# Optimization experiments

Measured on AMD Instinct MI355X. Metric: run time of the kernel, lower is better.

The kernel has to match this reference:

```python
import jax, jax.numpy as jnp
import numpy as np

B, N, F, F_PRIME, H = 16, 256, 64, 16, 128  # H = hidden width hardcoded as 128 in source


def _pairwise_dist(r):
    # torch.cdist(r, r), p=2. r: [B,N,3] -> [B,N,N]
    diff = r[:, :, None, :] - r[:, None, :, :]          # [B,N,N,3]
    sq = jnp.sum(diff * diff, axis=-1)                  # [B,N,N]
    safe = jnp.where(sq > 0, sq, 1.0)
    return jnp.where(sq > 0, jnp.sqrt(safe), 0.0)


def setup_inputs() -> dict:
    key = jax.random.key(0)
    ks = jax.random.split(key, 10)
    s = lambda fan_in: 1.0 / np.sqrt(fan_in)
    return {
        "r_batch": jax.random.uniform(ks[0], (B, N, 3), jnp.float32),
        "f_batch": jax.random.uniform(ks[1], (B, N, F), jnp.float32),
        # MessagePassingLayer MLP: 1 -> 128 -> F (weights stored [in, out])
        "mp_w1": jax.random.uniform(ks[2], (1, H), jnp.float32, -s(1), s(1)),
        "mp_b1": jax.random.uniform(ks[3], (H,), jnp.float32, -s(1), s(1)),
        "mp_w2": jax.random.uniform(ks[4], (H, F), jnp.float32, -s(H), s(H)),
        "mp_b2": jax.random.uniform(ks[5], (F,), jnp.float32, -s(H), s(H)),
        # PointwiseConvolutionLayer MLP: F -> 128 -> F_prime
        "pc_w1": jax.random.uniform(ks[6], (F, H), jnp.float32, -s(F), s(F)),
        "pc_b1": jax.random.uniform(ks[7], (H,), jnp.float32, -s(F), s(F)),
        "pc_w2": jax.random.uniform(ks[8], (H, F_PRIME), jnp.float32, -s(H), s(H)),
        "pc_b2": jax.random.uniform(ks[9], (F_PRIME,), jnp.float32, -s(H), s(H)),
    }


def reference(r_batch, f_batch, mp_w1, mp_b1, mp_w2, mp_b2, pc_w1, pc_b1, pc_w2, pc_b2):
    sp = jax.nn.softplus
    d = _pairwise_dist(r_batch)                                   # [B,N,N]
    # per-pair MLP on scalar distance: 1 -> 128 -> F
    hidden = sp(d[..., None] * mp_w1[0] + mp_b1)                  # [B,N,N,H]
    d_prime = sp(jnp.einsum('bijh,hf->bijf', hidden, mp_w2) + mp_b2)  # [B,N,N,F]
    # matmul + diagonal == per-feature weighted sum over neighbors j
    f_bar = sp(jnp.einsum('bijf,bjf->bif', d_prime, f_batch))     # [B,N,F]
    # pointwise MLP: F -> 128 -> F_prime
    h2 = sp(jnp.einsum('bnf,fh->bnh', f_bar, pc_w1) + pc_b1)      # [B,N,H]
    return sp(jnp.einsum('bnh,hp->bnp', h2, pc_w2) + pc_b2)       # [B,N,F_prime]
```

## Files before the change

### kernel.cpp

```cpp
#include <hip/hip_runtime.h>
#include <math.h>

#define B_   16
#define N_   256
#define F_   64
#define FP_  16
#define H_   128
#define K_   14
#define M_   64
#define DMAX 1.7320508075688772f
#define PI_F 3.14159265358979323846f
#define LROW 264
#define HP   136
#define FBP  72
#define MP   72

typedef _Float16 h16;
typedef __attribute__((ext_vector_type(2))) _Float16 h16x2;
typedef __attribute__((ext_vector_type(4))) _Float16 h16x4;
typedef __attribute__((ext_vector_type(8))) _Float16 h16x8;
typedef __attribute__((ext_vector_type(4))) float    f32x4;

__device__ __forceinline__ float sp(float x) {
    return fmaxf(x, 0.0f) + __logf(1.0f + __expf(-fabsf(x)));
}

__global__ __launch_bounds__(512) void pp_fused(
        const float* __restrict__ r,     const float* __restrict__ fb,
        const float* __restrict__ mp_w1, const float* __restrict__ mp_b1,
        const float* __restrict__ mp_w2, const float* __restrict__ mp_b2,
        const float* __restrict__ pc_w1, const float* __restrict__ pc_b1,
        const float* __restrict__ pc_w2, const float* __restrict__ pc_b2,
        float* __restrict__ out) {
    const int tid  = threadIdx.x;
    const int b    = blockIdx.x >> 4;
    const int i0   = (blockIdx.x & 15) << 4;
    const int wv   = tid >> 6;
    const int lane = tid & 63;
    const int ln   = lane & 15;
    const int q    = lane >> 4;

    __shared__ __align__(16) h16 s_hidA[64 * HP];
    __shared__ __align__(16) h16 s_w2T [F_ * HP];
    __shared__ __align__(16) h16 s_valsT[F_ * MP];
    __shared__ __align__(16) h16 s_fbT [F_ * LROW];
    __shared__ __align__(16) h16 s_xs  [16 * LROW];
    __shared__ float s_c  [K_ * F_];
    __shared__ h16   s_w1B[H_ * FBP];
    __shared__ h16   s_w2B[FP_ * HP];
    __shared__ h16   s_fbA[16 * FBP];
    __shared__ h16   s_h2A[16 * HP];
    __shared__ float s_ri [48];
    float* s_part = (float*)s_hidA;

    const int st = tid & 255;
    const int f4 = st & 15;
    const int jp = st >> 4;
    float4 pf0[8], pf1[8];
    float xj = 0.f, yj = 0.f, zj = 0.f;
    if (wv >= 4) {
        const float* fbb = fb + (size_t)b * N_ * F_;
        #pragma unroll
        for (int jb = 0; jb < 8; ++jb) {
            const int j0 = jb * 32 + jp * 2;
            pf0[jb] = *(const float4*)(fbb + (size_t)j0 * F_ + f4 * 4);
            pf1[jb] = *(const float4*)(fbb + (size_t)(j0 + 1) * F_ + f4 * 4);
        }
        xj = r[((size_t)b * N_ + st) * 3 + 0];
        yj = r[((size_t)b * N_ + st) * 3 + 1];
        zj = r[((size_t)b * N_ + st) * 3 + 2];
    }

    if (tid < 48) s_ri[tid] = r[((size_t)b * N_ + i0) * 3 + tid];
    #pragma unroll
    for (int e = 0; e < 4; ++e) {
        const int idx = e * 512 + tid;
        const int f = idx >> 5, h4 = idx & 31;
        const float4 v = *(const float4*)(pc_w1 + f * H_ + h4 * 4);
        s_w1B[(h4 * 4 + 0) * FBP + f] = (h16)v.x;
        s_w1B[(h4 * 4 + 1) * FBP + f] = (h16)v.y;
        s_w1B[(h4 * 4 + 2) * FBP + f] = (h16)v.z;
        s_w1B[(h4 * 4 + 3) * FBP + f] = (h16)v.w;
    }
    #pragma unroll
    for (int e = 0; e < 4; ++e) {
        const int idx = e * 512 + tid;
        const int h = idx >> 4, p = idx & 15;
        s_w2B[p * HP + h] = (h16)pc_w2[idx];
    }
    #pragma unroll
    for (int e = 0; e < 4; ++e) {
        const int idx = e * 512 + tid;
        const int h = idx >> 4, ff4 = idx & 15;
        const float4 v = *(const float4*)(mp_w2 + h * F_ + ff4 * 4);
        s_w2T[(ff4 * 4 + 0) * HP + h] = (h16)v.x;
        s_w2T[(ff4 * 4 + 1) * HP + h] = (h16)v.y;
        s_w2T[(ff4 * 4 + 2) * HP + h] = (h16)v.z;
        s_w2T[(ff4 * 4 + 3) * HP + h] = (h16)v.w;
    }
    {
        const int m  = tid >> 3;
        const int h0 = (tid & 7) * 16;
        const float th = PI_F * ((float)m + 0.5f) / (float)M_;
        const float d  = (__cosf(th) + 1.0f) * 0.5f * DMAX;
        #pragma unroll
        for (int hq = 0; hq < 4; ++hq) {
            const float4 w  = *(const float4*)(mp_w1 + h0 + hq * 4);
            const float4 bb = *(const float4*)(mp_b1 + h0 + hq * 4);
            h16x4 hv;
            hv.x = (h16)sp(fmaf(d, w.x, bb.x));
            hv.y = (h16)sp(fmaf(d, w.y, bb.y));
            hv.z = (h16)sp(fmaf(d, w.z, bb.z));
            hv.w = (h16)sp(fmaf(d, w.w, bb.w));
            *(h16x4*)&s_hidA[m * HP + h0 + hq * 4] = hv;
        }
    }
    __syncthreads();

    if (wv < 4) {
        f32x4 vacc[4];
        #pragma unroll
        for (int ft = 0; ft < 4; ++ft) vacc[ft] = (f32x4){0.f, 0.f, 0.f, 0.f};
        #pragma unroll
        for (int ks = 0; ks < 4; ++ks) {
            const h16x8 af = *(const h16x8*)&s_hidA[(wv * 16 + ln) * HP + ks * 32 + q * 8];
            #pragma unroll
            for (int ft = 0; ft < 4; ++ft) {
                const h16x8 bf = *(const h16x8*)&s_w2T[(ft * 16 + ln) * HP + ks * 32 + q * 8];
                vacc[ft] = __builtin_amdgcn_mfma_f32_16x16x32_f16(af, bf, vacc[ft], 0, 0, 0);
            }
        }
        #pragma unroll
        for (int ft = 0; ft < 4; ++ft) {
            const float b2v = mp_b2[ft * 16 + ln];
            const float vv[4] = {vacc[ft].x, vacc[ft].y, vacc[ft].z, vacc[ft].w};
            #pragma unroll
            for (int rr = 0; rr < 4; ++rr)
                s_valsT[(ft * 16 + ln) * MP + wv * 16 + q * 4 + rr] = (h16)sp(vv[rr] + b2v);
        }
    } else {
        #pragma unroll
        for (int jb = 0; jb < 8; ++jb) {
            const int j0 = jb * 32 + jp * 2;
            const float a0[4] = {pf0[jb].x, pf0[jb].y, pf0[jb].z, pf0[jb].w};
            const float a1[4] = {pf1[jb].x, pf1[jb].y, pf1[jb].z, pf1[jb].w};
            #pragma unroll
            for (int ff = 0; ff < 4; ++ff) {
                h16x2 pk; pk.x = (h16)a0[ff]; pk.y = (h16)a1[ff];
                *(h16x2*)&s_fbT[(f4 * 4 + ff) * LROW + j0] = pk;
            }
        }
    }
    __syncthreads();

    if (wv < 4) {
        f32x4 cacc = (f32x4){0.f, 0.f, 0.f, 0.f};
        #pragma unroll
        for (int cc = 0; cc < 2; ++cc) {
            const h16x8 af = *(const h16x8*)&s_valsT[(wv * 16 + ln) * MP + cc * 32 + q * 8];
            h16x8 bf;
            #pragma unroll
            for (int e = 0; e < 8; ++e) {
                const int m = cc * 32 + q * 8 + e;
                const float th = PI_F * ((float)m + 0.5f) / (float)M_;
                bf[e] = (h16)__cosf((float)ln * th);
            }
            cacc = __builtin_amdgcn_mfma_f32_16x16x32_f16(af, bf, cacc, 0, 0, 0);
        }
        if (ln < K_) {
            const float scale = ((ln == 0) ? 1.0f : 2.0f) / (float)M_;
            const float cv[4] = {cacc.x, cacc.y, cacc.z, cacc.w};
            #pragma unroll
            for (int rr = 0; rr < 4; ++rr)
                s_c[ln * F_ + wv * 16 + q * 4 + rr] = scale * cv[rr];
        }
    } else {
        const float sc = 2.0f / DMAX;
        #pragma unroll
        for (int m = 0; m < 16; ++m) {
            const float dx = s_ri[m * 3 + 0] - xj;
            const float dy = s_ri[m * 3 + 1] - yj;
            const float dz = s_ri[m * 3 + 2] - zj;
            const float sq = fmaf(dx, dx, fmaf(dy, dy, dz * dz));
            const float d  = sq > 0.0f ? sqrtf(sq) : 0.0f;
            s_xs[m * LROW + st] = (h16)(fmaf(d, sc, -1.0f));
        }
    }
    __syncthreads();

    const int j0 = wv * 32 + q * 8;
    const h16x8 x8 = *(const h16x8*)&s_xs[ln * LROW + j0];
    h16x8 bfrag[4];
    #pragma unroll
    for (int ft = 0; ft < 4; ++ft)
        bfrag[ft] = *(const h16x8*)&s_fbT[(ft * 16 + ln) * LROW + j0];

    h16x8 ones, twox, ta, tb;
    #pragma unroll
    for (int e = 0; e < 8; ++e) ones[e] = (h16)1.0f;
    twox = x8 + x8;
    ta = ones;
    tb = x8;

    f32x4 facc[4];
    #pragma unroll
    for (int ft = 0; ft < 4; ++ft) facc[ft] = (f32x4){0.f, 0.f, 0.f, 0.f};
    const f32x4 z4 = (f32x4){0.f, 0.f, 0.f, 0.f};

    for (int k = 0; k < K_; ++k) {
        #pragma unroll
        for (int ft = 0; ft < 4; ++ft) {
            const f32x4 a2 = __builtin_amdgcn_mfma_f32_16x16x32_f16(ta, bfrag[ft], z4, 0, 0, 0);
            const float ck = s_c[k * F_ + ft * 16 + ln];
            facc[ft].x = fmaf(ck, a2.x, facc[ft].x);
            facc[ft].y = fmaf(ck, a2.y, facc[ft].y);
            facc[ft].z = fmaf(ck, a2.z, facc[ft].z);
            facc[ft].w = fmaf(ck, a2.w, facc[ft].w);
        }
        const h16x8 tn = twox * tb - ta;
        ta = tb;
        tb = tn;
    }

    #pragma unroll
    for (int ft = 0; ft < 4; ++ft) {
        const float v[4] = {facc[ft].x, facc[ft].y, facc[ft].z, facc[ft].w};
        #pragma unroll
        for (int rr = 0; rr < 4; ++rr)
            s_part[(wv * 16 + q * 4 + rr) * 68 + ft * 16 + ln] = v[rr];
    }
    __syncthreads();

    #pragma unroll
    for (int e = 0; e < 2; ++e) {
        const int item = e * 512 + tid;
        const int i = item >> 6, f = item & 63;
        float s = 0.0f;
        #pragma unroll
        for (int g = 0; g < 8; ++g)
            s += s_part[(g * 16 + i) * 68 + f];
        s_fbA[i * FBP + f] = (h16)sp(s);
    }
    __syncthreads();

    {
        const int nt = wv;
        f32x4 hacc = (f32x4){0.f, 0.f, 0.f, 0.f};
        #pragma unroll
        for (int ks = 0; ks < 2; ++ks) {
            const h16x8 af = *(const h16x8*)&s_fbA[ln * FBP + ks * 32 + q * 8];
            const h16x8 bf = *(const h16x8*)&s_w1B[(nt * 16 + ln) * FBP + ks * 32 + q * 8];
            hacc = __builtin_amdgcn_mfma_f32_16x16x32_f16(af, bf, hacc, 0, 0, 0);
        }
        const float b1v = pc_b1[nt * 16 + ln];
        const float hv[4] = {hacc.x, hacc.y, hacc.z, hacc.w};
        #pragma unroll
        for (int rr = 0; rr < 4; ++rr)
            s_h2A[(q * 4 + rr) * HP + nt * 16 + ln] = (h16)sp(hv[rr] + b1v);
    }
    __syncthreads();

    {
        f32x4 oacc = (f32x4){0.f, 0.f, 0.f, 0.f};
        #pragma unroll
        for (int ks = 0; ks < 4; ++ks) {
            const h16x8 af = *(const h16x8*)&s_h2A[ln * HP + ks * 32 + q * 8];
            const h16x8 bf = *(const h16x8*)&s_w2B[ln * HP + ks * 32 + q * 8];
            oacc = __builtin_amdgcn_mfma_f32_16x16x32_f16(af, bf, oacc, 0, 0, 0);
        }
        if (wv == 0) {
            const float b2v = pc_b2[ln];
            const float ov[4] = {oacc.x, oacc.y, oacc.z, oacc.w};
            #pragma unroll
            for (int rr = 0; rr < 4; ++rr)
                out[((size_t)(b * N_ + i0 + q * 4 + rr)) * FP_ + ln] = sp(ov[rr] + b2v);
        }
    }
}

extern "C" void kernel_launch(void* const* d_in, const int* in_sizes, int n_in,
                              void* d_out, int out_size, void* d_ws, size_t ws_size,
                              hipStream_t stream) {
    const float* r_batch = (const float*)d_in[0];
    const float* f_batch = (const float*)d_in[1];
    const float* mp_w1   = (const float*)d_in[2];
    const float* mp_b1   = (const float*)d_in[3];
    const float* mp_w2   = (const float*)d_in[4];
    const float* mp_b2   = (const float*)d_in[5];
    const float* pc_w1   = (const float*)d_in[6];
    const float* pc_b1   = (const float*)d_in[7];
    const float* pc_w2   = (const float*)d_in[8];
    const float* pc_b2   = (const float*)d_in[9];
    float* out = (float*)d_out;

    pp_fused<<<B_ * (N_ / 16), 512, 0, stream>>>(
        r_batch, f_batch, mp_w1, mp_b1, mp_w2, mp_b2,
        pc_w1, pc_b1, pc_w2, pc_b2, out);
}
```

Measured before the change: 81.55 us.

## Double block to 1024 threads and split work across sixteen waves

Raises the block size from 512 to 1024 threads and redistributes every stage across 16 wavefronts. Each wave of the Chebyshev MFMA loop now handles 2 feature tiles instead of 4. The value MFMA, f_batch transpose, distance computation and partial-sum reduction are split across more waves. The aim is to shorten the per-block critical path, since the 256 blocks give only about one block per CU. In exchange there are fewer registers per thread, some waves sit idle in certain phases, and synchronising 1024 threads costs more.

```diff
diff --git a/kernel.cpp b/kernel.cpp
--- a/kernel.cpp
+++ b/kernel.cpp
@@ -25,7 +25,7 @@
     return fmaxf(x, 0.0f) + __logf(1.0f + __expf(-fabsf(x)));
 }
 
-__global__ __launch_bounds__(512) void pp_fused(
+__global__ __launch_bounds__(1024) void pp_fused(
         const float* __restrict__ r,     const float* __restrict__ fb,
         const float* __restrict__ mp_w1, const float* __restrict__ mp_b1,
         const float* __restrict__ mp_w2, const float* __restrict__ mp_b2,
@@ -53,28 +53,29 @@
     __shared__ float s_ri [48];
     float* s_part = (float*)s_hidA;
 
-    const int st = tid & 255;
+    const int st = tid & 511;
     const int f4 = st & 15;
     const int jp = st >> 4;
-    float4 pf0[8], pf1[8];
+    float4 pf0[4], pf1[4];
     float xj = 0.f, yj = 0.f, zj = 0.f;
-    if (wv >= 4) {
+    if (wv >= 8) {
         const float* fbb = fb + (size_t)b * N_ * F_;
         #pragma unroll
-        for (int jb = 0; jb < 8; ++jb) {
-            const int j0 = jb * 32 + jp * 2;
+        for (int jb = 0; jb < 4; ++jb) {
+            const int j0 = jb * 64 + jp * 2;
             pf0[jb] = *(const float4*)(fbb + (size_t)j0 * F_ + f4 * 4);
             pf1[jb] = *(const float4*)(fbb + (size_t)(j0 + 1) * F_ + f4 * 4);
         }
-        xj = r[((size_t)b * N_ + st) * 3 + 0];
-        yj = r[((size_t)b * N_ + st) * 3 + 1];
-        zj = r[((size_t)b * N_ + st) * 3 + 2];
+        const int lj = st & 255;
+        xj = r[((size_t)b * N_ + lj) * 3 + 0];
+        yj = r[((size_t)b * N_ + lj) * 3 + 1];
+        zj = r[((size_t)b * N_ + lj) * 3 + 2];
     }
 
     if (tid < 48) s_ri[tid] = r[((size_t)b * N_ + i0) * 3 + tid];
     #pragma unroll
-    for (int e = 0; e < 4; ++e) {
-        const int idx = e * 512 + tid;
+    for (int e = 0; e < 2; ++e) {
+        const int idx = e * 1024 + tid;
         const int f = idx >> 5, h4 = idx & 31;
         const float4 v = *(const float4*)(pc_w1 + f * H_ + h4 * 4);
         s_w1B[(h4 * 4 + 0) * FBP + f] = (h16)v.x;
@@ -83,14 +84,14 @@
         s_w1B[(h4 * 4 + 3) * FBP + f] = (h16)v.w;
     }
     #pragma unroll
-    for (int e = 0; e < 4; ++e) {
-        const int idx = e * 512 + tid;
+    for (int e = 0; e < 2; ++e) {
+        const int idx = e * 1024 + tid;
         const int h = idx >> 4, p = idx & 15;
         s_w2B[p * HP + h] = (h16)pc_w2[idx];
     }
     #pragma unroll
-    for (int e = 0; e < 4; ++e) {
-        const int idx = e * 512 + tid;
+    for (int e = 0; e < 2; ++e) {
+        const int idx = e * 1024 + tid;
         const int h = idx >> 4, ff4 = idx & 15;
         const float4 v = *(const float4*)(mp_w2 + h * F_ + ff4 * 4);
         s_w2T[(ff4 * 4 + 0) * HP + h] = (h16)v.x;
@@ -99,12 +100,12 @@
         s_w2T[(ff4 * 4 + 3) * HP + h] = (h16)v.w;
     }
     {
-        const int m  = tid >> 3;
-        const int h0 = (tid & 7) * 16;
+        const int m  = tid >> 4;
+        const int h0 = (tid & 15) * 8;
         const float th = PI_F * ((float)m + 0.5f) / (float)M_;
         const float d  = (__cosf(th) + 1.0f) * 0.5f * DMAX;
         #pragma unroll
-        for (int hq = 0; hq < 4; ++hq) {
+        for (int hq = 0; hq < 2; ++hq) {
             const float4 w  = *(const float4*)(mp_w1 + h0 + hq * 4);
             const float4 bb = *(const float4*)(mp_b1 + h0 + hq * 4);
             h16x4 hv;
@@ -117,31 +118,34 @@
     }
     __syncthreads();
 
-    if (wv < 4) {
-        f32x4 vacc[4];
-        #pragma unroll
-        for (int ft = 0; ft < 4; ++ft) vacc[ft] = (f32x4){0.f, 0.f, 0.f, 0.f};
+    if (wv < 8) {
+        const int mt = wv & 3, fg = wv >> 2;
+        f32x4 vacc[2];
+        #pragma unroll
+        for (int t = 0; t < 2; ++t) vacc[t] = (f32x4){0.f, 0.f, 0.f, 0.f};
         #pragma unroll
         for (int ks = 0; ks < 4; ++ks) {
-            const h16x8 af = *(const h16x8*)&s_hidA[(wv * 16 + ln) * HP + ks * 32 + q * 8];
-            #pragma unroll
-            for (int ft = 0; ft < 4; ++ft) {
+            const h16x8 af = *(const h16x8*)&s_hidA[(mt * 16 + ln) * HP + ks * 32 + q * 8];
+            #pragma unroll
+            for (int t = 0; t < 2; ++t) {
+                const int ft = fg * 2 + t;
                 const h16x8 bf = *(const h16x8*)&s_w2T[(ft * 16 + ln) * HP + ks * 32 + q * 8];
-                vacc[ft] = __builtin_amdgcn_mfma_f32_16x16x32_f16(af, bf, vacc[ft], 0, 0, 0);
+                vacc[t] = __builtin_amdgcn_mfma_f32_16x16x32_f16(af, bf, vacc[t], 0, 0, 0);
             }
         }
         #pragma unroll
-        for (int ft = 0; ft < 4; ++ft) {
+        for (int t = 0; t < 2; ++t) {
+            const int ft = fg * 2 + t;
             const float b2v = mp_b2[ft * 16 + ln];
-            const float vv[4] = {vacc[ft].x, vacc[ft].y, vacc[ft].z, vacc[ft].w};
+            const float vv[4] = {vacc[t].x, vacc[t].y, vacc[t].z, vacc[t].w};
             #pragma unroll
             for (int rr = 0; rr < 4; ++rr)
-                s_valsT[(ft * 16 + ln) * MP + wv * 16 + q * 4 + rr] = (h16)sp(vv[rr] + b2v);
+                s_valsT[(ft * 16 + ln) * MP + mt * 16 + q * 4 + rr] = (h16)sp(vv[rr] + b2v);
         }
     } else {
         #pragma unroll
-        for (int jb = 0; jb < 8; ++jb) {
-            const int j0 = jb * 32 + jp * 2;
+        for (int jb = 0; jb < 4; ++jb) {
+            const int j0 = jb * 64 + jp * 2;
             const float a0[4] = {pf0[jb].x, pf0[jb].y, pf0[jb].z, pf0[jb].w};
             const float a1[4] = {pf1[jb].x, pf1[jb].y, pf1[jb].z, pf1[jb].w};
             #pragma unroll
@@ -174,26 +178,30 @@
             for (int rr = 0; rr < 4; ++rr)
                 s_c[ln * F_ + wv * 16 + q * 4 + rr] = scale * cv[rr];
         }
-    } else {
+    } else if (wv >= 8) {
+        const int lj   = st & 255;
+        const int half = st >> 8;
         const float sc = 2.0f / DMAX;
         #pragma unroll
-        for (int m = 0; m < 16; ++m) {
+        for (int mm = 0; mm < 8; ++mm) {
+            const int m = half * 8 + mm;
             const float dx = s_ri[m * 3 + 0] - xj;
             const float dy = s_ri[m * 3 + 1] - yj;
             const float dz = s_ri[m * 3 + 2] - zj;
             const float sq = fmaf(dx, dx, fmaf(dy, dy, dz * dz));
             const float d  = sq > 0.0f ? sqrtf(sq) : 0.0f;
-            s_xs[m * LROW + st] = (h16)(fmaf(d, sc, -1.0f));
-        }
-    }
-    __syncthreads();
-
-    const int j0 = wv * 32 + q * 8;
+            s_xs[m * LROW + lj] = (h16)(fmaf(d, sc, -1.0f));
+        }
+    }
+    __syncthreads();
+
+    const int jw = wv & 7, fg = wv >> 3;
+    const int j0 = jw * 32 + q * 8;
     const h16x8 x8 = *(const h16x8*)&s_xs[ln * LROW + j0];
-    h16x8 bfrag[4];
-    #pragma unroll
-    for (int ft = 0; ft < 4; ++ft)
-        bfrag[ft] = *(const h16x8*)&s_fbT[(ft * 16 + ln) * LROW + j0];
+    h16x8 bfrag[2];
+    #pragma unroll
+    for (int t = 0; t < 2; ++t)
+        bfrag[t] = *(const h16x8*)&s_fbT[((fg * 2 + t) * 16 + ln) * LROW + j0];
 
     h16x8 ones, twox, ta, tb;
     #pragma unroll
@@ -202,20 +210,20 @@
     ta = ones;
     tb = x8;
 
-    f32x4 facc[4];
-    #pragma unroll
-    for (int ft = 0; ft < 4; ++ft) facc[ft] = (f32x4){0.f, 0.f, 0.f, 0.f};
+    f32x4 facc[2];
+    #pragma unroll
+    for (int t = 0; t < 2; ++t) facc[t] = (f32x4){0.f, 0.f, 0.f, 0.f};
     const f32x4 z4 = (f32x4){0.f, 0.f, 0.f, 0.f};
 
     for (int k = 0; k < K_; ++k) {
         #pragma unroll
-        for (int ft = 0; ft < 4; ++ft) {
-            const f32x4 a2 = __builtin_amdgcn_mfma_f32_16x16x32_f16(ta, bfrag[ft], z4, 0, 0, 0);
-            const float ck = s_c[k * F_ + ft * 16 + ln];
-            facc[ft].x = fmaf(ck, a2.x, facc[ft].x);
-            facc[ft].y = fmaf(ck, a2.y, facc[ft].y);
-            facc[ft].z = fmaf(ck, a2.z, facc[ft].z);
-            facc[ft].w = fmaf(ck, a2.w, facc[ft].w);
+        for (int t = 0; t < 2; ++t) {
+            const f32x4 a2 = __builtin_amdgcn_mfma_f32_16x16x32_f16(ta, bfrag[t], z4, 0, 0, 0);
+            const float ck = s_c[k * F_ + (fg * 2 + t) * 16 + ln];
+            facc[t].x = fmaf(ck, a2.x, facc[t].x);
+            facc[t].y = fmaf(ck, a2.y, facc[t].y);
+            facc[t].z = fmaf(ck, a2.z, facc[t].z);
+            facc[t].w = fmaf(ck, a2.w, facc[t].w);
         }
         const h16x8 tn = twox * tb - ta;
         ta = tb;
@@ -223,18 +231,16 @@
     }
 
     #pragma unroll
-    for (int ft = 0; ft < 4; ++ft) {
-        const float v[4] = {facc[ft].x, facc[ft].y, facc[ft].z, facc[ft].w};
+    for (int t = 0; t < 2; ++t) {
+        const float v[4] = {facc[t].x, facc[t].y, facc[t].z, facc[t].w};
         #pragma unroll
         for (int rr = 0; rr < 4; ++rr)
-            s_part[(wv * 16 + q * 4 + rr) * 68 + ft * 16 + ln] = v[rr];
-    }
-    __syncthreads();
-
-    #pragma unroll
-    for (int e = 0; e < 2; ++e) {
-        const int item = e * 512 + tid;
-        const int i = item >> 6, f = item & 63;
+            s_part[(jw * 16 + q * 4 + rr) * 68 + (fg * 2 + t) * 16 + ln] = v[rr];
+    }
+    __syncthreads();
+
+    {
+        const int i = tid >> 6, f = tid & 63;
         float s = 0.0f;
         #pragma unroll
         for (int g = 0; g < 8; ++g)
@@ -243,7 +249,7 @@
     }
     __syncthreads();
 
-    {
+    if (wv < 8) {
         const int nt = wv;
         f32x4 hacc = (f32x4){0.f, 0.f, 0.f, 0.f};
         #pragma unroll
@@ -260,7 +266,7 @@
     }
     __syncthreads();
 
-    {
+    if (wv == 0) {
         f32x4 oacc = (f32x4){0.f, 0.f, 0.f, 0.f};
         #pragma unroll
         for (int ks = 0; ks < 4; ++ks) {
@@ -268,13 +274,11 @@
             const h16x8 bf = *(const h16x8*)&s_w2B[ln * HP + ks * 32 + q * 8];
             oacc = __builtin_amdgcn_mfma_f32_16x16x32_f16(af, bf, oacc, 0, 0, 0);
         }
-        if (wv == 0) {
-            const float b2v = pc_b2[ln];
-            const float ov[4] = {oacc.x, oacc.y, oacc.z, oacc.w};
-            #pragma unroll
-            for (int rr = 0; rr < 4; ++rr)
-                out[((size_t)(b * N_ + i0 + q * 4 + rr)) * FP_ + ln] = sp(ov[rr] + b2v);
-        }
+        const float b2v = pc_b2[ln];
+        const float ov[4] = {oacc.x, oacc.y, oacc.z, oacc.w};
+        #pragma unroll
+        for (int rr = 0; rr < 4; ++rr)
+            out[((size_t)(b * N_ + i0 + q * 4 + rr)) * FP_ + ln] = sp(ov[rr] + b2v);
     }
 }
 
@@ -293,7 +297,7 @@
     const float* pc_b2   = (const float*)d_in[9];
     float* out = (float*)d_out;
 
-    pp_fused<<<B_ * (N_ / 16), 512, 0, stream>>>(
+    pp_fused<<<B_ * (N_ / 16), 1024, 0, stream>>>(
         r_batch, f_batch, mp_w1, mp_b1, mp_w2, mp_b2,
         pc_w1, pc_b1, pc_w2, pc_b2, out);
 }
```

After: 81.02 us, median of 2. Within noise of the previous version (-0.6%).

## Alias shared buffers in an arena and spread prologue work across all waves

Applied to the files above, without the earlier changes.

Replaces the separate shared-memory arrays with one aliased arena, so buffers used in different phases (hidden/w2T vs fbT/xs) share storage and LDS per block drops. The f_batch prefetch, transpose and distance computation are split across all 8 waves instead of only the upper 4, and the first MFMA stage is divided by feature groups so every wave participates. Launch bounds now request 4 blocks per CU, and the last MFMA is limited to wave 0. Aliasing requires extra barriers between phases, and the register cap may cause spills.

```diff
diff --git a/kernel.cpp b/kernel.cpp
--- a/kernel.cpp
+++ b/kernel.cpp
@@ -25,7 +25,7 @@
     return fmaxf(x, 0.0f) + __logf(1.0f + __expf(-fabsf(x)));
 }
 
-__global__ __launch_bounds__(512) void pp_fused(
+__global__ __launch_bounds__(512, 4) void pp_fused(
         const float* __restrict__ r,     const float* __restrict__ fb,
         const float* __restrict__ mp_w1, const float* __restrict__ mp_b1,
         const float* __restrict__ mp_w2, const float* __restrict__ mp_b2,
@@ -40,36 +40,37 @@
     const int ln   = lane & 15;
     const int q    = lane >> 4;
 
-    __shared__ __align__(16) h16 s_hidA[64 * HP];
-    __shared__ __align__(16) h16 s_w2T [F_ * HP];
-    __shared__ __align__(16) h16 s_valsT[F_ * MP];
-    __shared__ __align__(16) h16 s_fbT [F_ * LROW];
-    __shared__ __align__(16) h16 s_xs  [16 * LROW];
+    __shared__ __align__(16) char s_arena[44032];
     __shared__ float s_c  [K_ * F_];
     __shared__ h16   s_w1B[H_ * FBP];
     __shared__ h16   s_w2B[FP_ * HP];
     __shared__ h16   s_fbA[16 * FBP];
     __shared__ h16   s_h2A[16 * HP];
     __shared__ float s_ri [48];
-    float* s_part = (float*)s_hidA;
-
-    const int st = tid & 255;
-    const int f4 = st & 15;
-    const int jp = st >> 4;
-    float4 pf0[8], pf1[8];
-    float xj = 0.f, yj = 0.f, zj = 0.f;
-    if (wv >= 4) {
+
+    h16*   s_hidA  = (h16*)s_arena;
+    h16*   s_w2T   = (h16*)(s_arena + 17408);
+    h16*   s_valsT = (h16*)(s_arena + 34816);
+    h16*   s_fbT   = (h16*)s_arena;
+    h16*   s_xs    = (h16*)(s_arena + 33792);
+    float* s_part  = (float*)s_arena;
+
+    const int f4 = tid & 15;
+    const int jp = tid >> 4;
+    float4 pf0[4], pf1[4];
+    {
         const float* fbb = fb + (size_t)b * N_ * F_;
         #pragma unroll
-        for (int jb = 0; jb < 8; ++jb) {
-            const int j0 = jb * 32 + jp * 2;
+        for (int jb = 0; jb < 4; ++jb) {
+            const int j0 = jb * 64 + jp * 2;
             pf0[jb] = *(const float4*)(fbb + (size_t)j0 * F_ + f4 * 4);
             pf1[jb] = *(const float4*)(fbb + (size_t)(j0 + 1) * F_ + f4 * 4);
         }
-        xj = r[((size_t)b * N_ + st) * 3 + 0];
-        yj = r[((size_t)b * N_ + st) * 3 + 1];
-        zj = r[((size_t)b * N_ + st) * 3 + 2];
-    }
+    }
+    const int lj = tid & 255;
+    const float xj = r[((size_t)b * N_ + lj) * 3 + 0];
+    const float yj = r[((size_t)b * N_ + lj) * 3 + 1];
+    const float zj = r[((size_t)b * N_ + lj) * 3 + 2];
 
     if (tid < 48) s_ri[tid] = r[((size_t)b * N_ + i0) * 3 + tid];
     #pragma unroll
@@ -117,38 +118,29 @@
     }
     __syncthreads();
 
-    if (wv < 4) {
-        f32x4 vacc[4];
-        #pragma unroll
-        for (int ft = 0; ft < 4; ++ft) vacc[ft] = (f32x4){0.f, 0.f, 0.f, 0.f};
+    {
+        const int mt = wv & 3, fg = wv >> 2;
+        f32x4 vacc[2];
+        #pragma unroll
+        for (int t = 0; t < 2; ++t) vacc[t] = (f32x4){0.f, 0.f, 0.f, 0.f};
         #pragma unroll
         for (int ks = 0; ks < 4; ++ks) {
-            const h16x8 af = *(const h16x8*)&s_hidA[(wv * 16 + ln) * HP + ks * 32 + q * 8];
+            const h16x8 af = *(const h16x8*)&s_hidA[(mt * 16 + ln) * HP + ks * 32 + q * 8];
             #pragma unroll
-            for (int ft = 0; ft < 4; ++ft) {
+            for (int t = 0; t < 2; ++t) {
+                const int ft = fg * 2 + t;
                 const h16x8 bf = *(const h16x8*)&s_w2T[(ft * 16 + ln) * HP + ks * 32 + q * 8];
-                vacc[ft] = __builtin_amdgcn_mfma_f32_16x16x32_f16(af, bf, vacc[ft], 0, 0, 0);
+                vacc[t] = __builtin_amdgcn_mfma_f32_16x16x32_f16(af, bf, vacc[t], 0, 0, 0);
             }
         }
         #pragma unroll
-        for (int ft = 0; ft < 4; ++ft) {
+        for (int t = 0; t < 2; ++t) {
+            const int ft = fg * 2 + t;
             const float b2v = mp_b2[ft * 16 + ln];
-            const float vv[4] = {vacc[ft].x, vacc[ft].y, vacc[ft].z, vacc[ft].w};
+            const float vv[4] = {vacc[t].x, vacc[t].y, vacc[t].z, vacc[t].w};
             #pragma unroll
             for (int rr = 0; rr < 4; ++rr)
-                s_valsT[(ft * 16 + ln) * MP + wv * 16 + q * 4 + rr] = (h16)sp(vv[rr] + b2v);
-        }
-    } else {
-        #pragma unroll
-        for (int jb = 0; jb < 8; ++jb) {
-            const int j0 = jb * 32 + jp * 2;
-            const float a0[4] = {pf0[jb].x, pf0[jb].y, pf0[jb].z, pf0[jb].w};
-            const float a1[4] = {pf1[jb].x, pf1[jb].y, pf1[jb].z, pf1[jb].w};
-            #pragma unroll
-            for (int ff = 0; ff < 4; ++ff) {
-                h16x2 pk; pk.x = (h16)a0[ff]; pk.y = (h16)a1[ff];
-                *(h16x2*)&s_fbT[(f4 * 4 + ff) * LROW + j0] = pk;
-            }
+                s_valsT[(ft * 16 + ln) * MP + mt * 16 + q * 4 + rr] = (h16)sp(vv[rr] + b2v);
         }
     }
     __syncthreads();
@@ -174,16 +166,32 @@
             for (int rr = 0; rr < 4; ++rr)
                 s_c[ln * F_ + wv * 16 + q * 4 + rr] = scale * cv[rr];
         }
-    } else {
+    }
+    #pragma unroll
+    for (int jb = 0; jb < 4; ++jb) {
+        const int j0 = jb * 64 + jp * 2;
+        const float a0[4] = {pf0[jb].x, pf0[jb].y, pf0[jb].z, pf0[jb].w};
+        const float a1[4] = {pf1[jb].x, pf1[jb].y, pf1[jb].z, pf1[jb].w};
+        #pragma unroll
+        for (int ff = 0; ff < 4; ++ff) {
+            h16x2 pk; pk.x = (h16)a0[ff]; pk.y = (h16)a1[ff];
+            *(h16x2*)&s_fbT[(f4 * 4 + ff) * LROW + j0] = pk;
+        }
+    }
+    __syncthreads();
+
+    {
+        const int half = tid >> 8;
         const float sc = 2.0f / DMAX;
         #pragma unroll
-        for (int m = 0; m < 16; ++m) {
+        for (int mm = 0; mm < 8; ++mm) {
+            const int m = half * 8 + mm;
             const float dx = s_ri[m * 3 + 0] - xj;
             const float dy = s_ri[m * 3 + 1] - yj;
             const float dz = s_ri[m * 3 + 2] - zj;
             const float sq = fmaf(dx, dx, fmaf(dy, dy, dz * dz));
             const float d  = sq > 0.0f ? sqrtf(sq) : 0.0f;
-            s_xs[m * LROW + st] = (h16)(fmaf(d, sc, -1.0f));
+            s_xs[m * LROW + lj] = (h16)(fmaf(d, sc, -1.0f));
         }
     }
     __syncthreads();
@@ -194,6 +202,7 @@
     #pragma unroll
     for (int ft = 0; ft < 4; ++ft)
         bfrag[ft] = *(const h16x8*)&s_fbT[(ft * 16 + ln) * LROW + j0];
+    __syncthreads();
 
     h16x8 ones, twox, ta, tb;
     #pragma unroll
@@ -260,7 +269,7 @@
     }
     __syncthreads();
 
-    {
+    if (wv == 0) {
         f32x4 oacc = (f32x4){0.f, 0.f, 0.f, 0.f};
         #pragma unroll
         for (int ks = 0; ks < 4; ++ks) {
@@ -268,13 +277,11 @@
             const h16x8 bf = *(const h16x8*)&s_w2B[ln * HP + ks * 32 + q * 8];
             oacc = __builtin_amdgcn_mfma_f32_16x16x32_f16(af, bf, oacc, 0, 0, 0);
         }
-        if (wv == 0) {
-            const float b2v = pc_b2[ln];
-            const float ov[4] = {oacc.x, oacc.y, oacc.z, oacc.w};
-            #pragma unroll
-            for (int rr = 0; rr < 4; ++rr)
-                out[((size_t)(b * N_ + i0 + q * 4 + rr)) * FP_ + ln] = sp(ov[rr] + b2v);
-        }
+        const float b2v = pc_b2[ln];
+        const float ov[4] = {oacc.x, oacc.y, oacc.z, oacc.w};
+        #pragma unroll
+        for (int rr = 0; rr < 4; ++rr)
+            out[((size_t)(b * N_ + i0 + q * 4 + rr)) * FP_ + ln] = sp(ov[rr] + b2v);
     }
 }
 
```

Measured after the change: 84.44 us. +3.5%, slower.
